# Optimization experiments

Measured on AMD Instinct MI355X. Metric: run time of the kernel, lower is better.

The kernel has to match this reference:

```python
import jax, jax.numpy as jnp
import numpy as np

N_NODES = 100000
N_EDGES = 1000000
D = 64  # gat_input_size == gat_hidden_size
NEG_SLOPE = 0.2  # PyG GATConv default leaky_relu slope


def setup_inputs() -> dict:
    key = jax.random.key(0)
    k1, k2, k3, k4, k5, k6 = jax.random.split(key, 6)
    g = jax.random.normal(k1, (N_NODES, D), dtype=jnp.float32)
    edge_index = jax.random.randint(k2, (2, N_EDGES), 0, N_NODES, dtype=jnp.int32)
    scale = 1.0 / np.sqrt(D)
    W = jax.random.normal(k3, (D, D), dtype=jnp.float32) * scale
    att_src = jax.random.normal(k4, (D,), dtype=jnp.float32) * scale
    att_dst = jax.random.normal(k5, (D,), dtype=jnp.float32) * scale
    bias = jnp.zeros((D,), dtype=jnp.float32)
    return {"g": g, "edge_index": edge_index, "W": W,
            "att_src": att_src, "att_dst": att_dst, "bias": bias}


def _gat_layer(x, src, dst, W, att_src, att_dst, bias):
    N = x.shape[0]
    h = x @ W                               # [N, D] projected features
    a_src = h @ att_src                     # [N] per-node source logits
    a_dst = h @ att_dst                     # [N] per-node target logits
    e = jax.nn.leaky_relu(a_src[src] + a_dst[dst], NEG_SLOPE)  # [E]
    # numerically stable segment softmax over edges grouped by target node
    m = jax.ops.segment_max(e, dst, num_segments=N)            # [N]
    m = jnp.where(jnp.isfinite(m), m, 0.0)                     # isolated nodes
    ex = jnp.exp(e - m[dst])                                   # [E]
    denom = jax.ops.segment_sum(ex, dst, num_segments=N)       # [N]
    alpha = ex / (denom[dst] + 1e-16)                          # [E]
    out = jax.ops.segment_sum(alpha[:, None] * h[src], dst, num_segments=N)
    return out + bias


def reference(g, edge_index, W, att_src, att_dst, bias):
    src, dst = edge_index[0], edge_index[1]
    for _ in range(4):  # same shared GAT applied 4 times
        g = _gat_layer(g, src, dst, W, att_src, att_dst, bias)
    return g
```

## Files before the change

kernel.cpp:

```cpp
#include <hip/hip_runtime.h>
#include <hip/hip_bf16.h>

typedef unsigned int u32;
typedef unsigned short u16;
typedef unsigned long long u64;
typedef __attribute__((ext_vector_type(8))) short short8;
typedef __attribute__((ext_vector_type(4))) float f32x4;
typedef __attribute__((ext_vector_type(2))) float f32x2;

#define LRELU_SLOPE 0.2f
#define BPB 32
#define MAXPER 13000

__device__ inline float bfbits(u32 hi) { union { u32 i; float f; } v; v.i = hi; return v.f; }
__device__ inline float bflo(u32 w) { return bfbits(w << 16); }
__device__ inline float bfhi(u32 w) { return bfbits(w & 0xFFFF0000u); }
__device__ inline float bf2f(u16 s) { return bfbits(((u32)s) << 16); }
__device__ inline u16 f2bf(float f) {
  union { float f; u32 i; } v; v.f = f;
  u32 r = v.i + 0x7FFFu + ((v.i >> 16) & 1u);
  return (u16)(r >> 16);
}
__device__ inline f32x2 up2(u32 w) { return (f32x2){bflo(w), bfhi(w)}; }

__global__ void dp_kernel(const u32* __restrict__ g, int nwords, int* __restrict__ mode,
                          const void* __restrict__ W, const void* __restrict__ as,
                          const void* __restrict__ ad, const void* __restrict__ bs,
                          float* __restrict__ pf, u16* __restrict__ wfrag,
                          int* __restrict__ gcnt) {
  __shared__ int cnt;
  if (threadIdx.x == 0) cnt = 0;
  if (threadIdx.x < 8) gcnt[threadIdx.x] = 0;
  __syncthreads();
  int c = 0;
  for (int i = threadIdx.x; i < nwords; i += 256) {
    u32 e = g[i] & 0x7F80u;
    if (e >= 0x3000u && e <= 0x4180u) c++;
  }
  atomicAdd(&cnt, c);
  __syncthreads();
  int md = (2 * cnt > nwords) ? 1 : 0;
  if (threadIdx.x == 0) *mode = md;

  for (int i = threadIdx.x; i < 4288; i += 256) {
    const void* p; int j;
    if (i < 4096)      { p = W;  j = i; }
    else if (i < 4160) { p = as; j = i - 4096; }
    else if (i < 4224) { p = ad; j = i - 4160; }
    else               { p = bs; j = i - 4224; }
    pf[i] = md ? bf2f(((const u16*)p)[j]) : ((const float*)p)[j];
  }
  __syncthreads();
  for (int i = threadIdx.x; i < 4096; i += 256) {
    int f = i >> 9, lane = (i >> 3) & 63, j = i & 7;
    int cc = f >> 1, t = f & 1;
    int k = 32 * t + 8 * (lane >> 4) + j;
    int n = 16 * cc + (lane & 15);
    wfrag[i] = f2bf(pf[k * 64 + n]);
  }
}

__global__ void __launch_bounds__(256) binA_kernel(
    const int* __restrict__ src, const int* __restrict__ dst, int* __restrict__ gcnt,
    uint2* __restrict__ binned, int E, int nper, int cap) {
  __shared__ int lcnt[8], lbase[8], lcur[8];
  const int K = 8;
  int tile0 = blockIdx.x * (256 * K);
  int t = threadIdx.x;
  if (t < 8) { lcnt[t] = 0; lcur[t] = 0; }
  __syncthreads();
  int dv[K], sv[K], bv[K];
#pragma unroll
  for (int j = 0; j < K; ++j) {
    int idx = tile0 + j * 256 + t;
    bool ok = idx < E;
    int d = ok ? __builtin_nontemporal_load(&dst[idx]) : 0;
    int s = ok ? __builtin_nontemporal_load(&src[idx]) : 0;
    int b = -1;
    if (ok) {
      b = (d >= 4 * nper) ? 4 : 0;
      if (d >= (b + 2) * nper) b += 2;
      if (d >= (b + 1) * nper) b += 1;
      atomicAdd(&lcnt[b], 1);
    }
    dv[j] = d; sv[j] = s; bv[j] = b;
  }
  __syncthreads();
  if (t < 8) lbase[t] = atomicAdd(&gcnt[t], lcnt[t]);
  __syncthreads();
#pragma unroll
  for (int j = 0; j < K; ++j) {
    int b = bv[j];
    if (b >= 0) {
      int slot = lbase[b] + atomicAdd(&lcur[b], 1);
      if (slot < cap) binned[(size_t)b * cap + slot] = make_uint2((u32)sv[j], (u32)dv[j]);
    }
  }
}

__global__ void __launch_bounds__(256) histA_kernel(
    const uint2* __restrict__ binned, const int* __restrict__ gcnt,
    u32* __restrict__ slices, int nper, int cap) {
  __shared__ u32 cnt_lds[MAXPER];
  int b = blockIdx.x & 7;
  int j = blockIdx.x >> 3;
  int cnt = gcnt[b]; if (cnt > cap) cnt = cap;
  int chunk = (cnt + BPB - 1) / BPB;
  int begin = j * chunk;
  int endc = begin + chunk; if (endc > cnt) endc = cnt;
  for (int k = threadIdx.x; k < nper; k += 256) cnt_lds[k] = 0;
  __syncthreads();
  const uint2* reg = binned + (size_t)b * cap;
  int kbase = b * nper;
  for (int i = begin + threadIdx.x; i < endc; i += 256)
    atomicAdd(&cnt_lds[(int)reg[i].y - kbase], 1u);
  __syncthreads();
  u32* out = slices + (size_t)(b * BPB + j) * nper;
  for (int k = threadIdx.x; k < nper; k += 256) out[k] = cnt_lds[k];
}

__global__ void scan1f_kernel(const u32* __restrict__ slices, int* __restrict__ row_off,
                              int* __restrict__ partials, int nper, int N) {
  __shared__ int smem[1024];
  int t = threadIdx.x;
  int idx = blockIdx.x * 1024 + t;
  int v = 0;
  if (idx < N) {
    int b = idx / nper;
    int kk = idx - b * nper;
    const u32* s = slices + (size_t)b * BPB * nper + kk;
    u32 tt = 0;
#pragma unroll 8
    for (int j = 0; j < BPB; ++j) tt += s[(size_t)j * nper];
    v = (int)((tt + 7u) & ~7u);
  }
  smem[t] = v;
  __syncthreads();
  for (int off = 1; off < 1024; off <<= 1) {
    int u = (t >= off) ? smem[t - off] : 0;
    __syncthreads();
    smem[t] += u;
    __syncthreads();
  }
  if (idx < N) row_off[idx + 1] = smem[t];
  if (t == 1023) partials[blockIdx.x] = smem[t];
}

__global__ void scan3c_kernel(int* __restrict__ row_off, const int* __restrict__ partials,
                              int P, u32* __restrict__ slices, int* __restrict__ csr_src,
                              int nper, int N, int dummy) {
  __shared__ int smem[1024];
  int t = threadIdx.x;
  int pv = (t < P) ? partials[t] : 0;
  smem[t] = pv;
  __syncthreads();
  for (int off = 1; off < 1024; off <<= 1) {
    int u = (t >= off) ? smem[t - off] : 0;
    __syncthreads();
    smem[t] += u;
    __syncthreads();
  }
  int blk = blockIdx.x;
  int prefix = (blk > 0) ? smem[blk - 1] : 0;
  int idx = blk * 1024 + t;
  if (idx == 0) row_off[0] = 0;
  if (idx < N) {
    int vend = row_off[idx + 1] + prefix;
    row_off[idx + 1] = vend;
    int b = idx / nper;
    int kk = idx - b * nper;
    u32* s = slices + (size_t)b * BPB * nper + kk;
    u32 tv[BPB];
    u32 deg = 0;
#pragma unroll
    for (int j = 0; j < BPB; ++j) { tv[j] = s[(size_t)j * nper]; deg += tv[j]; }
    u32 pdeg = (deg + 7u) & ~7u;
    u32 run = (u32)vend - pdeg;
#pragma unroll
    for (int j = 0; j < BPB; ++j) { s[(size_t)j * nper] = run; run += tv[j]; }
    for (u32 p = run; p < (u32)vend; ++p) csr_src[p] = dummy;
  }
}

__global__ void __launch_bounds__(256) scatterB_kernel(
    const uint2* __restrict__ binned, const int* __restrict__ gcnt,
    const u32* __restrict__ slices, int* __restrict__ csr_src, int nper, int cap) {
  __shared__ u32 base_lds[MAXPER];
  int b = blockIdx.x & 7;
  int j = blockIdx.x >> 3;
  int cnt = gcnt[b]; if (cnt > cap) cnt = cap;
  int chunk = (cnt + BPB - 1) / BPB;
  int begin = j * chunk;
  int endc = begin + chunk; if (endc > cnt) endc = cnt;
  const u32* s = slices + (size_t)(b * BPB + j) * nper;
  for (int k = threadIdx.x; k < nper; k += 256) base_lds[k] = s[k];
  __syncthreads();
  const uint2* reg = binned + (size_t)b * cap;
  int kbase = b * nper;
  for (int i = begin + threadIdx.x; i < endc; i += 256) {
    uint2 r = reg[i];
    u32 p = atomicAdd(&base_lds[(int)r.y - kbase], 1u);
    csr_src[p] = (int)r.x;
  }
}

__global__ void hist_local_kernel(const uint2* __restrict__ binned, const int* __restrict__ gcnt,
                                  int* __restrict__ deg, int cap) {
  int b = blockIdx.x & 7;
  int vb = blockIdx.x >> 3, nvb = gridDim.x >> 3;
  int cnt = gcnt[b]; if (cnt > cap) cnt = cap;
  const uint2* reg = binned + (size_t)b * cap;
  for (int i = vb * blockDim.x + threadIdx.x; i < cnt; i += nvb * blockDim.x)
    atomicAdd(&deg[reg[i].y], 1);
}

__global__ void scatter_local_kernel(const uint2* __restrict__ binned, const int* __restrict__ gcnt,
                                     int* __restrict__ cursor, int* __restrict__ csr_src, int cap) {
  int b = blockIdx.x & 7;
  int vb = blockIdx.x >> 3, nvb = gridDim.x >> 3;
  int cnt = gcnt[b]; if (cnt > cap) cnt = cap;
  const uint2* reg = binned + (size_t)b * cap;
  for (int i = vb * blockDim.x + threadIdx.x; i < cnt; i += nvb * blockDim.x) {
    uint2 r = reg[i];
    int p = atomicAdd(&cursor[r.y], 1);
    csr_src[p] = (int)r.x;
  }
}

__global__ void scan1_kernel(const int* __restrict__ deg, int* __restrict__ row_off,
                             int* __restrict__ partials, int N) {
  __shared__ int smem[1024];
  int t = threadIdx.x;
  int idx = blockIdx.x * 1024 + t;
  int v = (idx < N) ? (int)(((u32)deg[idx] + 7u) & ~7u) : 0;
  smem[t] = v;
  __syncthreads();
  for (int off = 1; off < 1024; off <<= 1) {
    int u = (t >= off) ? smem[t - off] : 0;
    __syncthreads();
    smem[t] += u;
    __syncthreads();
  }
  if (idx < N) row_off[idx + 1] = smem[t];
  if (t == 1023) partials[blockIdx.x] = smem[t];
}

__global__ void scan2_kernel(int* __restrict__ partials, int P) {
  __shared__ int smem[1024];
  int t = threadIdx.x;
  int v = (t < P) ? partials[t] : 0;
  smem[t] = v;
  __syncthreads();
  for (int off = 1; off < 1024; off <<= 1) {
    int u = (t >= off) ? smem[t - off] : 0;
    __syncthreads();
    smem[t] += u;
    __syncthreads();
  }
  if (t < P) partials[t] = smem[t];
}

__global__ void scan3_kernel(int* __restrict__ row_off, const int* __restrict__ partials,
                             int* __restrict__ cursor, int N) {
  int b = blockIdx.x;
  int idx = b * 1024 + threadIdx.x;
  if (idx < N) {
    int v = row_off[idx + 1] + ((b > 0) ? partials[b - 1] : 0);
    row_off[idx + 1] = v;
    if (idx + 1 < N) cursor[idx + 1] = v;
  }
  if (idx == 0) { row_off[0] = 0; cursor[0] = 0; }
}

__global__ void padC_kernel(const int* __restrict__ row_off, const int* __restrict__ cursor,
                            int* __restrict__ csr_src, int N, int dummy) {
  int i = blockIdx.x * blockDim.x + threadIdx.x;
  if (i >= N) return;
  int e = row_off[i + 1];
  for (int p = cursor[i]; p < e; ++p) csr_src[p] = dummy;
}

__global__ void __launch_bounds__(256) proj0_kernel(
    const void* __restrict__ graw, const int* __restrict__ mode,
    const u16* __restrict__ wfrag, const float* __restrict__ pf,
    u16* __restrict__ h0, u16* __restrict__ h1,
    float* __restrict__ as0, float* __restrict__ as1,
    float* __restrict__ ad0, int N) {
  if (blockIdx.x == 0) {
    if (threadIdx.x < 32)       ((u32*)(h0 + (size_t)N * 64))[threadIdx.x] = 0u;
    else if (threadIdx.x < 64)  ((u32*)(h1 + (size_t)N * 64))[threadIdx.x - 32] = 0u;
    else if (threadIdx.x == 64) as0[N] = -1e30f;
    else if (threadIdx.x == 65) as1[N] = -1e30f;
  }
  int lane = threadIdx.x & 63;
  int quad = lane >> 4, m = lane & 15;
  int wtile = (int)((blockIdx.x * (size_t)blockDim.x + threadIdx.x) >> 6);
  int ntiles = (N + 15) >> 4;
  int nwaves = (int)((gridDim.x * (size_t)blockDim.x) >> 6);

  int md = *mode;
  bool f32in = (md == 0);

  short8 bfrag[8];
#pragma unroll
  for (int f = 0; f < 8; ++f)
    bfrag[f] = *(const short8*)(wfrag + f * 512 + lane * 8);
  float asv[4], adv[4];
#pragma unroll
  for (int c = 0; c < 4; ++c) {
    asv[c] = pf[4096 + 16 * c + m];
    adv[c] = pf[4160 + 16 * c + m];
  }

  for (int tile = wtile; tile < ntiles; tile += nwaves) {
    int row0 = tile << 4;
    int rl = row0 + m; if (rl > N - 1) rl = N - 1;
    short8 a0, a1;
    if (f32in) {
      const float* xr = (const float*)graw + (size_t)rl * 64 + 8 * quad;
      float4 f0 = *(const float4*)(xr);
      float4 f1 = *(const float4*)(xr + 4);
      float4 f2 = *(const float4*)(xr + 32);
      float4 f3 = *(const float4*)(xr + 36);
      a0[0] = (short)f2bf(f0.x); a0[1] = (short)f2bf(f0.y);
      a0[2] = (short)f2bf(f0.z); a0[3] = (short)f2bf(f0.w);
      a0[4] = (short)f2bf(f1.x); a0[5] = (short)f2bf(f1.y);
      a0[6] = (short)f2bf(f1.z); a0[7] = (short)f2bf(f1.w);
      a1[0] = (short)f2bf(f2.x); a1[1] = (short)f2bf(f2.y);
      a1[2] = (short)f2bf(f2.z); a1[3] = (short)f2bf(f2.w);
      a1[4] = (short)f2bf(f3.x); a1[5] = (short)f2bf(f3.y);
      a1[6] = (short)f2bf(f3.z); a1[7] = (short)f2bf(f3.w);
    } else {
      const u16* xr = (const u16*)graw + (size_t)rl * 64 + 8 * quad;
      a0 = *(const short8*)(xr);
      a1 = *(const short8*)(xr + 32);
    }

    f32x4 acc[4];
#pragma unroll
    for (int c = 0; c < 4; ++c) {
      f32x4 z = {0.f, 0.f, 0.f, 0.f};
      z = __builtin_amdgcn_mfma_f32_16x16x32_bf16(a0, bfrag[2 * c + 0], z, 0, 0, 0);
      z = __builtin_amdgcn_mfma_f32_16x16x32_bf16(a1, bfrag[2 * c + 1], z, 0, 0, 0);
      acc[c] = z;
    }

#pragma unroll
    for (int r = 0; r < 4; ++r) {
      int row = row0 + 4 * quad + r;
      float v0 = acc[0][r], v1 = acc[1][r], v2 = acc[2][r], v3 = acc[3][r];
      if (row < N) {
        u16* hr = h0 + (size_t)row * 64 + m;
        hr[0]  = f2bf(v0);
        hr[16] = f2bf(v1);
        hr[32] = f2bf(v2);
        hr[48] = f2bf(v3);
      }
      float s1 = v0 * asv[0] + v1 * asv[1] + v2 * asv[2] + v3 * asv[3];
      float s2 = v0 * adv[0] + v1 * adv[1] + v2 * adv[2] + v3 * adv[3];
#pragma unroll
      for (int msk = 1; msk <= 8; msk <<= 1) {
        s1 += __shfl_xor(s1, msk, 64);
        s2 += __shfl_xor(s2, msk, 64);
      }
      if (m == 0 && row < N) { as0[row] = s1; ad0[row] = s2; }
    }
  }
}

__global__ void __launch_bounds__(256) fusedFG_kernel(
    const u16* __restrict__ hin, const float* __restrict__ asi,
    const float* __restrict__ adi, u16* __restrict__ hout,
    float* __restrict__ aso, float* __restrict__ ado,
    const int* __restrict__ row_off, const int* __restrict__ csr_src,
    const float* __restrict__ pf, const u16* __restrict__ wfrag, int N) {
  __shared__ u16 xs[16][72];
  __shared__ float sred[2][16][4];

  int tid = threadIdx.x;
  int lane = tid & 63;
  int w = tid >> 6;
  int quad = lane >> 4, m = lane & 15;
  int grp = lane >> 4;
  int eg = (lane >> 3) & 1;
  int fg = lane & 7;
  int tile = blockIdx.x;
  int row_in = w * 4 + grp;
  int i = tile * 16 + row_in;
  bool valid = i < N;

  short8 bf0 = *(const short8*)(wfrag + (2 * w + 0) * 512 + lane * 8);
  short8 bf1 = *(const short8*)(wfrag + (2 * w + 1) * 512 + lane * 8);
  float asw = pf[4096 + 16 * w + m];
  float adw = pf[4160 + 16 * w + m];

  int beg = 0, end = 0;
  float advv = 0.f;
  if (valid) { beg = row_off[i]; end = row_off[i + 1]; advv = adi[i]; }

  f32x2 acc0 = {0.f, 0.f}, acc1 = {0.f, 0.f}, acc2 = {0.f, 0.f}, acc3 = {0.f, 0.f};
  float den = 0.f;
  for (int b0 = beg; b0 < end; b0 += 8) {
    int eA = b0 + eg;
    int sA = csr_src[eA];
    int sB = csr_src[eA + 2];
    int sC = csr_src[eA + 4];
    int sD = csr_src[eA + 6];
    float aA = asi[sA];
    float aB = asi[sB];
    float aC = asi[sC];
    float aD = asi[sD];
    uint4 hA = ((const uint4*)(hin + (size_t)sA * 64))[fg];
    uint4 hB = ((const uint4*)(hin + (size_t)sB * 64))[fg];
    uint4 hC = ((const uint4*)(hin + (size_t)sC * 64))[fg];
    uint4 hD = ((const uint4*)(hin + (size_t)sD * 64))[fg];

    float tA = aA + advv; tA = (tA > 0.f) ? tA : LRELU_SLOPE * tA;
    float tB = aB + advv; tB = (tB > 0.f) ? tB : LRELU_SLOPE * tB;
    float tC = aC + advv; tC = (tC > 0.f) ? tC : LRELU_SLOPE * tC;
    float tD = aD + advv; tD = (tD > 0.f) ? tD : LRELU_SLOPE * tD;
    float wA = __expf(fminf(tA, 60.f));
    float wB = __expf(fminf(tB, 60.f));
    float wC = __expf(fminf(tC, 60.f));
    float wD = __expf(fminf(tD, 60.f));
    den += (wA + wB) + (wC + wD);
    f32x2 wA2 = {wA, wA}, wB2 = {wB, wB}, wC2 = {wC, wC}, wD2 = {wD, wD};
    acc0 += wA2 * up2(hA.x); acc0 += wB2 * up2(hB.x);
    acc0 += wC2 * up2(hC.x); acc0 += wD2 * up2(hD.x);
    acc1 += wA2 * up2(hA.y); acc1 += wB2 * up2(hB.y);
    acc1 += wC2 * up2(hC.y); acc1 += wD2 * up2(hD.y);
    acc2 += wA2 * up2(hA.z); acc2 += wB2 * up2(hB.z);
    acc2 += wC2 * up2(hC.z); acc2 += wD2 * up2(hD.z);
    acc3 += wA2 * up2(hA.w); acc3 += wB2 * up2(hB.w);
    acc3 += wC2 * up2(hC.w); acc3 += wD2 * up2(hD.w);
  }
  den += __shfl_xor(den, 8, 64);
#pragma unroll
  for (int c = 0; c < 2; ++c) {
    acc0[c] += __shfl_xor(acc0[c], 8, 64);
    acc1[c] += __shfl_xor(acc1[c], 8, 64);
    acc2[c] += __shfl_xor(acc2[c], 8, 64);
    acc3[c] += __shfl_xor(acc3[c], 8, 64);
  }
  float inv = (den > 0.f) ? 1.f / den : 0.f;
  float oa[8] = {acc0[0], acc0[1], acc1[0], acc1[1],
                 acc2[0], acc2[1], acc3[0], acc3[1]};

  if (!eg) {
    u32 o[4];
    if (valid) {
#pragma unroll
      for (int j = 0; j < 4; ++j) {
        float v0 = oa[2 * j]     * inv + pf[4224 + 8 * fg + 2 * j];
        float v1 = oa[2 * j + 1] * inv + pf[4224 + 8 * fg + 2 * j + 1];
        o[j] = (u32)f2bf(v0) | ((u32)f2bf(v1) << 16);
      }
    } else {
      o[0] = o[1] = o[2] = o[3] = 0u;
    }
    *(uint4*)&xs[row_in][fg * 8] = make_uint4(o[0], o[1], o[2], o[3]);
  }
  __syncthreads();

  short8 a0 = *(const short8*)&xs[m][8 * quad];
  short8 a1 = *(const short8*)&xs[m][32 + 8 * quad];
  f32x4 z = {0.f, 0.f, 0.f, 0.f};
  z = __builtin_amdgcn_mfma_f32_16x16x32_bf16(a0, bf0, z, 0, 0, 0);
  z = __builtin_amdgcn_mfma_f32_16x16x32_bf16(a1, bf1, z, 0, 0, 0);
#pragma unroll
  for (int r = 0; r < 4; ++r) {
    int row = tile * 16 + 4 * quad + r;
    if (row < N) hout[(size_t)row * 64 + 16 * w + m] = f2bf(z[r]);
    float s1 = z[r] * asw, s2 = z[r] * adw;
#pragma unroll
    for (int msk = 1; msk <= 8; msk <<= 1) {
      s1 += __shfl_xor(s1, msk, 64);
      s2 += __shfl_xor(s2, msk, 64);
    }
    if (m == 0) { sred[0][4 * quad + r][w] = s1; sred[1][4 * quad + r][w] = s2; }
  }
  __syncthreads();
  if (tid < 32) {
    int row = tid & 15, sel = tid >> 4;
    float v = sred[sel][row][0] + sred[sel][row][1] + sred[sel][row][2] + sred[sel][row][3];
    int gr = tile * 16 + row;
    if (gr < N) (sel ? ado : aso)[gr] = v;
  }
}

__global__ void __launch_bounds__(256) gatherL_kernel(
    const u16* __restrict__ h, const float* __restrict__ a_src,
    const float* __restrict__ a_dst, const int* __restrict__ row_off,
    const int* __restrict__ csr_src, const float* __restrict__ pf,
    void* __restrict__ dout, int N, const int* __restrict__ mode) {
  int lane = threadIdx.x & 63;
  int grp = lane >> 4;
  int eg  = (lane >> 3) & 1;
  int fg  = lane & 7;
  int wid = (int)((blockIdx.x * blockDim.x + threadIdx.x) >> 6);
  int i0 = wid * 4;
  if (i0 >= N) return;
  int i = i0 + grp;
  bool valid = i < N;

  int beg = 0, end = 0;
  float adv = 0.f;
  if (valid) {
    beg = row_off[i];
    end = row_off[i + 1];
    adv = a_dst[i];
  }

  f32x2 acc0 = {0.f, 0.f}, acc1 = {0.f, 0.f}, acc2 = {0.f, 0.f}, acc3 = {0.f, 0.f};
  float den = 0.f;

  for (int b0 = beg; b0 < end; b0 += 8) {
    int eA = b0 + eg;
    int sA = csr_src[eA];
    int sB = csr_src[eA + 2];
    int sC = csr_src[eA + 4];
    int sD = csr_src[eA + 6];
    float aA = a_src[sA];
    float aB = a_src[sB];
    float aC = a_src[sC];
    float aD = a_src[sD];
    uint4 hA = ((const uint4*)(h + (size_t)sA * 64))[fg];
    uint4 hB = ((const uint4*)(h + (size_t)sB * 64))[fg];
    uint4 hC = ((const uint4*)(h + (size_t)sC * 64))[fg];
    uint4 hD = ((const uint4*)(h + (size_t)sD * 64))[fg];

    float tA = aA + adv; tA = (tA > 0.f) ? tA : LRELU_SLOPE * tA;
    float tB = aB + adv; tB = (tB > 0.f) ? tB : LRELU_SLOPE * tB;
    float tC = aC + adv; tC = (tC > 0.f) ? tC : LRELU_SLOPE * tC;
    float tD = aD + adv; tD = (tD > 0.f) ? tD : LRELU_SLOPE * tD;
    float wA = __expf(fminf(tA, 60.f));
    float wB = __expf(fminf(tB, 60.f));
    float wC = __expf(fminf(tC, 60.f));
    float wD = __expf(fminf(tD, 60.f));
    den += (wA + wB) + (wC + wD);
    f32x2 wA2 = {wA, wA}, wB2 = {wB, wB}, wC2 = {wC, wC}, wD2 = {wD, wD};
    acc0 += wA2 * up2(hA.x); acc0 += wB2 * up2(hB.x);
    acc0 += wC2 * up2(hC.x); acc0 += wD2 * up2(hD.x);
    acc1 += wA2 * up2(hA.y); acc1 += wB2 * up2(hB.y);
    acc1 += wC2 * up2(hC.y); acc1 += wD2 * up2(hD.y);
    acc2 += wA2 * up2(hA.z); acc2 += wB2 * up2(hB.z);
    acc2 += wC2 * up2(hC.z); acc2 += wD2 * up2(hD.z);
    acc3 += wA2 * up2(hA.w); acc3 += wB2 * up2(hB.w);
    acc3 += wC2 * up2(hC.w); acc3 += wD2 * up2(hD.w);
  }

  den += __shfl_xor(den, 8, 64);
#pragma unroll
  for (int c = 0; c < 2; ++c) {
    acc0[c] += __shfl_xor(acc0[c], 8, 64);
    acc1[c] += __shfl_xor(acc1[c], 8, 64);
    acc2[c] += __shfl_xor(acc2[c], 8, 64);
    acc3[c] += __shfl_xor(acc3[c], 8, 64);
  }
  float inv = (den > 0.f) ? 1.f / den : 0.f;

  if (!valid || eg) return;

  float oa[8] = {acc0[0], acc0[1], acc1[0], acc1[1], acc2[0], acc2[1], acc3[0], acc3[1]};
  if (*mode) {
    u32 o[4];
#pragma unroll
    for (int j = 0; j < 4; ++j) {
      float f0 = oa[2 * j]     * inv + pf[4224 + 8 * fg + 2 * j];
      float f1 = oa[2 * j + 1] * inv + pf[4224 + 8 * fg + 2 * j + 1];
      o[j] = (u32)f2bf(f0) | ((u32)f2bf(f1) << 16);
    }
    *(uint4*)((u16*)dout + (size_t)i * 64 + fg * 8) = make_uint4(o[0], o[1], o[2], o[3]);
  } else {
    float o[8];
#pragma unroll
    for (int j = 0; j < 8; ++j)
      o[j] = oa[j] * inv + pf[4224 + 8 * fg + j];
    float* dp = (float*)dout + (size_t)i * 64 + fg * 8;
    *(float4*)(dp)     = make_float4(o[0], o[1], o[2], o[3]);
    *(float4*)(dp + 4) = make_float4(o[4], o[5], o[6], o[7]);
  }
}

extern "C" void kernel_launch(void* const* d_in, const int* in_sizes, int n_in,
                              void* d_out, int out_size, void* d_ws, size_t ws_size,
                              hipStream_t stream) {
  const void* g     = d_in[0];
  const int*  edge  = (const int*)d_in[1];
  const void* Wp    = d_in[2];
  const void* attsp = d_in[3];
  const void* attdp = d_in[4];
  const void* biasp = d_in[5];

  const int D = 64;
  const int N = in_sizes[0] / D;
  const int E = in_sizes[1] / 2;
  const int* src = edge;
  const int* dst = edge + E;

  int nper = (N + 7) / 8;
  bool fast_csr = (nper <= MAXPER);

  char* ws = (char*)d_ws;
  size_t off = 0;
  auto alloc = [&](size_t bytes) -> char* {
    char* p = ws + off;
    off += (bytes + 255) & ~size_t(255);
    return p;
  };
  size_t h_bytes = (size_t)(N + 1) * D * sizeof(u16);
  size_t slice_bytes = (size_t)8 * BPB * nper * sizeof(u32);
  u16*   h0       = (u16*)alloc(h_bytes > slice_bytes ? h_bytes : slice_bytes);
  u16*   h1       = (u16*)alloc(h_bytes);
  u32*   slices   = (u32*)h0;
  float* pf       = (float*)alloc(4288 * sizeof(float));
  u16*   wfrag    = (u16*)alloc(4096 * sizeof(u16));
  float* as0      = (float*)alloc((size_t)(N + 1) * sizeof(float));
  float* as1      = (float*)alloc((size_t)(N + 1) * sizeof(float));
  float* ad0      = (float*)alloc((size_t)N * sizeof(float));
  float* ad1      = (float*)alloc((size_t)N * sizeof(float));
  int*   deg      = (int*)alloc((size_t)N * sizeof(int));
  int*   row_off  = (int*)alloc((size_t)(N + 1) * sizeof(int));
  int*   cursor   = (int*)alloc((size_t)N * sizeof(int));
  int*   csr_src  = (int*)alloc(((size_t)E + 8 * (size_t)N) * sizeof(int));
  int*   partials = (int*)alloc(1024 * sizeof(int));
  int*   mode     = (int*)alloc(256);
  int*   gcnt     = (int*)alloc(256);
  int    cap      = E / 8 + 16384;
  uint2* binned   = (uint2*)alloc((size_t)8 * cap * sizeof(uint2));

  dp_kernel<<<1, 256, 0, stream>>>((const u32*)g, 4096, mode, Wp, attsp, attdp, biasp,
                                   pf, wfrag, gcnt);

  if (!fast_csr) hipMemsetAsync(deg, 0, (size_t)N * sizeof(int), stream);
  int abl = (E + 2047) / 2048;
  binA_kernel<<<abl, 256, 0, stream>>>(src, dst, gcnt, binned, E, nper, cap);

  int nblk = (N + 1023) / 1024;
  if (fast_csr) {
    histA_kernel<<<8 * BPB, 256, 0, stream>>>(binned, gcnt, slices, nper, cap);
    scan1f_kernel<<<nblk, 1024, 0, stream>>>(slices, row_off, partials, nper, N);
    scan3c_kernel<<<nblk, 1024, 0, stream>>>(row_off, partials, nblk, slices, csr_src,
                                             nper, N, N);
    scatterB_kernel<<<8 * BPB, 256, 0, stream>>>(binned, gcnt, slices, csr_src, nper, cap);
  } else {
    hist_local_kernel<<<1024, 256, 0, stream>>>(binned, gcnt, deg, cap);
    scan1_kernel<<<nblk, 1024, 0, stream>>>(deg, row_off, partials, N);
    scan2_kernel<<<1, 1024, 0, stream>>>(partials, nblk);
    scan3_kernel<<<nblk, 1024, 0, stream>>>(row_off, partials, cursor, N);
    scatter_local_kernel<<<1024, 256, 0, stream>>>(binned, gcnt, cursor, csr_src, cap);
    padC_kernel<<<(N + 255) / 256, 256, 0, stream>>>(row_off, cursor, csr_src, N, N);
  }

  int ntiles = (N + 15) / 16;
  int tblocks = (ntiles + 3) / 4;

  proj0_kernel<<<tblocks, 256, 0, stream>>>(g, mode, wfrag, pf, h0, h1, as0, as1, ad0, N);

  fusedFG_kernel<<<ntiles, 256, 0, stream>>>(h0, as0, ad0, h1, as1, ad1,
                                             row_off, csr_src, pf, wfrag, N);
  fusedFG_kernel<<<ntiles, 256, 0, stream>>>(h1, as1, ad1, h0, as0, ad0,
                                             row_off, csr_src, pf, wfrag, N);
  fusedFG_kernel<<<ntiles, 256, 0, stream>>>(h0, as0, ad0, h1, as1, ad1,
                                             row_off, csr_src, pf, wfrag, N);

  gatherL_kernel<<<ntiles, 256, 0, stream>>>(h1, as1, ad1, row_off, csr_src, pf,
                                             d_out, N, mode);
}
```

Measured before the change: 267.8 us.

## Fuse edge binning with first projection and add XCD-aware tile swizzle

Edge binning and the layer-0 projection now run as one launch, with the block ranges split between the two jobs. This lets independent work overlap and removes a launch. To make that possible, the slices buffer no longer aliases h0 and gets its own allocation. The fused aggregation and final gather kernels remap block IDs so that consecutive tiles land on the same XCD, which should improve L2 locality. The gather kernel's indexing also changes to one 16-row tile per block. The cost is extra workspace memory and some imbalance between the two kinds of block inside the fused launch.

New measurement: 261.2 us (median of 2 runs). -2.5%, faster.

```diff
diff --git a/kernel.cpp b/kernel.cpp
--- a/kernel.cpp
+++ b/kernel.cpp
@@ -23,6 +23,12 @@
 }
 __device__ inline f32x2 up2(u32 w) { return (f32x2){bflo(w), bfhi(w)}; }
 
+__device__ inline int xcd_swz(int orig, int nwg) {
+  int xcd = orig & 7, idx = orig >> 3;
+  int q = nwg >> 3, r = nwg & 7;
+  return (xcd < r ? xcd * (q + 1) : r * (q + 1) + (xcd - r) * q) + idx;
+}
+
 __global__ void dp_kernel(const u32* __restrict__ g, int nwords, int* __restrict__ mode,
                           const void* __restrict__ W, const void* __restrict__ as,
                           const void* __restrict__ ad, const void* __restrict__ bs,
@@ -60,12 +66,12 @@
   }
 }
 
-__global__ void __launch_bounds__(256) binA_kernel(
-    const int* __restrict__ src, const int* __restrict__ dst, int* __restrict__ gcnt,
-    uint2* __restrict__ binned, int E, int nper, int cap) {
+__device__ void binA_body(const int* __restrict__ src, const int* __restrict__ dst,
+                          int* __restrict__ gcnt, uint2* __restrict__ binned,
+                          int E, int nper, int cap, int bid) {
   __shared__ int lcnt[8], lbase[8], lcur[8];
   const int K = 8;
-  int tile0 = blockIdx.x * (256 * K);
+  int tile0 = bid * (256 * K);
   int t = threadIdx.x;
   if (t < 8) { lcnt[t] = 0; lcur[t] = 0; }
   __syncthreads();
@@ -98,195 +104,12 @@
   }
 }
 
-__global__ void __launch_bounds__(256) histA_kernel(
-    const uint2* __restrict__ binned, const int* __restrict__ gcnt,
-    u32* __restrict__ slices, int nper, int cap) {
-  __shared__ u32 cnt_lds[MAXPER];
-  int b = blockIdx.x & 7;
-  int j = blockIdx.x >> 3;
-  int cnt = gcnt[b]; if (cnt > cap) cnt = cap;
-  int chunk = (cnt + BPB - 1) / BPB;
-  int begin = j * chunk;
-  int endc = begin + chunk; if (endc > cnt) endc = cnt;
-  for (int k = threadIdx.x; k < nper; k += 256) cnt_lds[k] = 0;
-  __syncthreads();
-  const uint2* reg = binned + (size_t)b * cap;
-  int kbase = b * nper;
-  for (int i = begin + threadIdx.x; i < endc; i += 256)
-    atomicAdd(&cnt_lds[(int)reg[i].y - kbase], 1u);
-  __syncthreads();
-  u32* out = slices + (size_t)(b * BPB + j) * nper;
-  for (int k = threadIdx.x; k < nper; k += 256) out[k] = cnt_lds[k];
-}
-
-__global__ void scan1f_kernel(const u32* __restrict__ slices, int* __restrict__ row_off,
-                              int* __restrict__ partials, int nper, int N) {
-  __shared__ int smem[1024];
-  int t = threadIdx.x;
-  int idx = blockIdx.x * 1024 + t;
-  int v = 0;
-  if (idx < N) {
-    int b = idx / nper;
-    int kk = idx - b * nper;
-    const u32* s = slices + (size_t)b * BPB * nper + kk;
-    u32 tt = 0;
-#pragma unroll 8
-    for (int j = 0; j < BPB; ++j) tt += s[(size_t)j * nper];
-    v = (int)((tt + 7u) & ~7u);
-  }
-  smem[t] = v;
-  __syncthreads();
-  for (int off = 1; off < 1024; off <<= 1) {
-    int u = (t >= off) ? smem[t - off] : 0;
-    __syncthreads();
-    smem[t] += u;
-    __syncthreads();
-  }
-  if (idx < N) row_off[idx + 1] = smem[t];
-  if (t == 1023) partials[blockIdx.x] = smem[t];
-}
-
-__global__ void scan3c_kernel(int* __restrict__ row_off, const int* __restrict__ partials,
-                              int P, u32* __restrict__ slices, int* __restrict__ csr_src,
-                              int nper, int N, int dummy) {
-  __shared__ int smem[1024];
-  int t = threadIdx.x;
-  int pv = (t < P) ? partials[t] : 0;
-  smem[t] = pv;
-  __syncthreads();
-  for (int off = 1; off < 1024; off <<= 1) {
-    int u = (t >= off) ? smem[t - off] : 0;
-    __syncthreads();
-    smem[t] += u;
-    __syncthreads();
-  }
-  int blk = blockIdx.x;
-  int prefix = (blk > 0) ? smem[blk - 1] : 0;
-  int idx = blk * 1024 + t;
-  if (idx == 0) row_off[0] = 0;
-  if (idx < N) {
-    int vend = row_off[idx + 1] + prefix;
-    row_off[idx + 1] = vend;
-    int b = idx / nper;
-    int kk = idx - b * nper;
-    u32* s = slices + (size_t)b * BPB * nper + kk;
-    u32 tv[BPB];
-    u32 deg = 0;
-#pragma unroll
-    for (int j = 0; j < BPB; ++j) { tv[j] = s[(size_t)j * nper]; deg += tv[j]; }
-    u32 pdeg = (deg + 7u) & ~7u;
-    u32 run = (u32)vend - pdeg;
-#pragma unroll
-    for (int j = 0; j < BPB; ++j) { s[(size_t)j * nper] = run; run += tv[j]; }
-    for (u32 p = run; p < (u32)vend; ++p) csr_src[p] = dummy;
-  }
-}
-
-__global__ void __launch_bounds__(256) scatterB_kernel(
-    const uint2* __restrict__ binned, const int* __restrict__ gcnt,
-    const u32* __restrict__ slices, int* __restrict__ csr_src, int nper, int cap) {
-  __shared__ u32 base_lds[MAXPER];
-  int b = blockIdx.x & 7;
-  int j = blockIdx.x >> 3;
-  int cnt = gcnt[b]; if (cnt > cap) cnt = cap;
-  int chunk = (cnt + BPB - 1) / BPB;
-  int begin = j * chunk;
-  int endc = begin + chunk; if (endc > cnt) endc = cnt;
-  const u32* s = slices + (size_t)(b * BPB + j) * nper;
-  for (int k = threadIdx.x; k < nper; k += 256) base_lds[k] = s[k];
-  __syncthreads();
-  const uint2* reg = binned + (size_t)b * cap;
-  int kbase = b * nper;
-  for (int i = begin + threadIdx.x; i < endc; i += 256) {
-    uint2 r = reg[i];
-    u32 p = atomicAdd(&base_lds[(int)r.y - kbase], 1u);
-    csr_src[p] = (int)r.x;
-  }
-}
-
-__global__ void hist_local_kernel(const uint2* __restrict__ binned, const int* __restrict__ gcnt,
-                                  int* __restrict__ deg, int cap) {
-  int b = blockIdx.x & 7;
-  int vb = blockIdx.x >> 3, nvb = gridDim.x >> 3;
-  int cnt = gcnt[b]; if (cnt > cap) cnt = cap;
-  const uint2* reg = binned + (size_t)b * cap;
-  for (int i = vb * blockDim.x + threadIdx.x; i < cnt; i += nvb * blockDim.x)
-    atomicAdd(&deg[reg[i].y], 1);
-}
-
-__global__ void scatter_local_kernel(const uint2* __restrict__ binned, const int* __restrict__ gcnt,
-                                     int* __restrict__ cursor, int* __restrict__ csr_src, int cap) {
-  int b = blockIdx.x & 7;
-  int vb = blockIdx.x >> 3, nvb = gridDim.x >> 3;
-  int cnt = gcnt[b]; if (cnt > cap) cnt = cap;
-  const uint2* reg = binned + (size_t)b * cap;
-  for (int i = vb * blockDim.x + threadIdx.x; i < cnt; i += nvb * blockDim.x) {
-    uint2 r = reg[i];
-    int p = atomicAdd(&cursor[r.y], 1);
-    csr_src[p] = (int)r.x;
-  }
-}
-
-__global__ void scan1_kernel(const int* __restrict__ deg, int* __restrict__ row_off,
-                             int* __restrict__ partials, int N) {
-  __shared__ int smem[1024];
-  int t = threadIdx.x;
-  int idx = blockIdx.x * 1024 + t;
-  int v = (idx < N) ? (int)(((u32)deg[idx] + 7u) & ~7u) : 0;
-  smem[t] = v;
-  __syncthreads();
-  for (int off = 1; off < 1024; off <<= 1) {
-    int u = (t >= off) ? smem[t - off] : 0;
-    __syncthreads();
-    smem[t] += u;
-    __syncthreads();
-  }
-  if (idx < N) row_off[idx + 1] = smem[t];
-  if (t == 1023) partials[blockIdx.x] = smem[t];
-}
-
-__global__ void scan2_kernel(int* __restrict__ partials, int P) {
-  __shared__ int smem[1024];
-  int t = threadIdx.x;
-  int v = (t < P) ? partials[t] : 0;
-  smem[t] = v;
-  __syncthreads();
-  for (int off = 1; off < 1024; off <<= 1) {
-    int u = (t >= off) ? smem[t - off] : 0;
-    __syncthreads();
-    smem[t] += u;
-    __syncthreads();
-  }
-  if (t < P) partials[t] = smem[t];
-}
-
-__global__ void scan3_kernel(int* __restrict__ row_off, const int* __restrict__ partials,
-                             int* __restrict__ cursor, int N) {
-  int b = blockIdx.x;
-  int idx = b * 1024 + threadIdx.x;
-  if (idx < N) {
-    int v = row_off[idx + 1] + ((b > 0) ? partials[b - 1] : 0);
-    row_off[idx + 1] = v;
-    if (idx + 1 < N) cursor[idx + 1] = v;
-  }
-  if (idx == 0) { row_off[0] = 0; cursor[0] = 0; }
-}
-
-__global__ void padC_kernel(const int* __restrict__ row_off, const int* __restrict__ cursor,
-                            int* __restrict__ csr_src, int N, int dummy) {
-  int i = blockIdx.x * blockDim.x + threadIdx.x;
-  if (i >= N) return;
-  int e = row_off[i + 1];
-  for (int p = cursor[i]; p < e; ++p) csr_src[p] = dummy;
-}
-
-__global__ void __launch_bounds__(256) proj0_kernel(
-    const void* __restrict__ graw, const int* __restrict__ mode,
-    const u16* __restrict__ wfrag, const float* __restrict__ pf,
-    u16* __restrict__ h0, u16* __restrict__ h1,
-    float* __restrict__ as0, float* __restrict__ as1,
-    float* __restrict__ ad0, int N) {
-  if (blockIdx.x == 0) {
+__device__ void proj0_body(const void* __restrict__ graw, const int* __restrict__ mode,
+                           const u16* __restrict__ wfrag, const float* __restrict__ pf,
+                           u16* __restrict__ h0, u16* __restrict__ h1,
+                           float* __restrict__ as0, float* __restrict__ as1,
+                           float* __restrict__ ad0, int N, int bid, int pblocks) {
+  if (bid == 0) {
     if (threadIdx.x < 32)       ((u32*)(h0 + (size_t)N * 64))[threadIdx.x] = 0u;
     else if (threadIdx.x < 64)  ((u32*)(h1 + (size_t)N * 64))[threadIdx.x - 32] = 0u;
     else if (threadIdx.x == 64) as0[N] = -1e30f;
@@ -294,9 +117,9 @@
   }
   int lane = threadIdx.x & 63;
   int quad = lane >> 4, m = lane & 15;
-  int wtile = (int)((blockIdx.x * (size_t)blockDim.x + threadIdx.x) >> 6);
+  int wtile = (int)(((size_t)bid * 256 + threadIdx.x) >> 6);
   int ntiles = (N + 15) >> 4;
-  int nwaves = (int)((gridDim.x * (size_t)blockDim.x) >> 6);
+  int nwaves = pblocks * 4;
 
   int md = *mode;
   bool f32in = (md == 0);
@@ -368,6 +191,219 @@
   }
 }
 
+__global__ void __launch_bounds__(256) fatBP_kernel(
+    const int* __restrict__ src, const int* __restrict__ dst, int* __restrict__ gcnt,
+    uint2* __restrict__ binned, int E, int nper, int cap, int abl,
+    const void* __restrict__ graw, const int* __restrict__ mode,
+    const u16* __restrict__ wfrag, const float* __restrict__ pf,
+    u16* __restrict__ h0, u16* __restrict__ h1,
+    float* __restrict__ as0, float* __restrict__ as1,
+    float* __restrict__ ad0, int N) {
+  if ((int)blockIdx.x < abl) {
+    binA_body(src, dst, gcnt, binned, E, nper, cap, (int)blockIdx.x);
+  } else {
+    proj0_body(graw, mode, wfrag, pf, h0, h1, as0, as1, ad0, N,
+               (int)blockIdx.x - abl, (int)gridDim.x - abl);
+  }
+}
+
+__global__ void __launch_bounds__(256) binA_kernel(
+    const int* __restrict__ src, const int* __restrict__ dst, int* __restrict__ gcnt,
+    uint2* __restrict__ binned, int E, int nper, int cap) {
+  binA_body(src, dst, gcnt, binned, E, nper, cap, (int)blockIdx.x);
+}
+__global__ void __launch_bounds__(256) proj0_kernel(
+    const void* __restrict__ graw, const int* __restrict__ mode,
+    const u16* __restrict__ wfrag, const float* __restrict__ pf,
+    u16* __restrict__ h0, u16* __restrict__ h1,
+    float* __restrict__ as0, float* __restrict__ as1,
+    float* __restrict__ ad0, int N) {
+  proj0_body(graw, mode, wfrag, pf, h0, h1, as0, as1, ad0, N,
+             (int)blockIdx.x, (int)gridDim.x);
+}
+
+__global__ void __launch_bounds__(256) histA_kernel(
+    const uint2* __restrict__ binned, const int* __restrict__ gcnt,
+    u32* __restrict__ slices, int nper, int cap) {
+  __shared__ u32 cnt_lds[MAXPER];
+  int b = blockIdx.x & 7;
+  int j = blockIdx.x >> 3;
+  int cnt = gcnt[b]; if (cnt > cap) cnt = cap;
+  int chunk = (cnt + BPB - 1) / BPB;
+  int begin = j * chunk;
+  int endc = begin + chunk; if (endc > cnt) endc = cnt;
+  for (int k = threadIdx.x; k < nper; k += 256) cnt_lds[k] = 0;
+  __syncthreads();
+  const uint2* reg = binned + (size_t)b * cap;
+  int kbase = b * nper;
+  for (int i = begin + threadIdx.x; i < endc; i += 256)
+    atomicAdd(&cnt_lds[(int)reg[i].y - kbase], 1u);
+  __syncthreads();
+  u32* out = slices + (size_t)(b * BPB + j) * nper;
+  for (int k = threadIdx.x; k < nper; k += 256) out[k] = cnt_lds[k];
+}
+
+__global__ void scan1f_kernel(const u32* __restrict__ slices, int* __restrict__ row_off,
+                              int* __restrict__ partials, int nper, int N) {
+  __shared__ int smem[1024];
+  int t = threadIdx.x;
+  int idx = blockIdx.x * 1024 + t;
+  int v = 0;
+  if (idx < N) {
+    int b = idx / nper;
+    int kk = idx - b * nper;
+    const u32* s = slices + (size_t)b * BPB * nper + kk;
+    u32 tt = 0;
+#pragma unroll 8
+    for (int j = 0; j < BPB; ++j) tt += s[(size_t)j * nper];
+    v = (int)((tt + 7u) & ~7u);
+  }
+  smem[t] = v;
+  __syncthreads();
+  for (int off = 1; off < 1024; off <<= 1) {
+    int u = (t >= off) ? smem[t - off] : 0;
+    __syncthreads();
+    smem[t] += u;
+    __syncthreads();
+  }
+  if (idx < N) row_off[idx + 1] = smem[t];
+  if (t == 1023) partials[blockIdx.x] = smem[t];
+}
+
+__global__ void scan3c_kernel(int* __restrict__ row_off, const int* __restrict__ partials,
+                              int P, u32* __restrict__ slices, int* __restrict__ csr_src,
+                              int nper, int N, int dummy) {
+  __shared__ int smem[1024];
+  int t = threadIdx.x;
+  int pv = (t < P) ? partials[t] : 0;
+  smem[t] = pv;
+  __syncthreads();
+  for (int off = 1; off < 1024; off <<= 1) {
+    int u = (t >= off) ? smem[t - off] : 0;
+    __syncthreads();
+    smem[t] += u;
+    __syncthreads();
+  }
+  int blk = blockIdx.x;
+  int prefix = (blk > 0) ? smem[blk - 1] : 0;
+  int idx = blk * 1024 + t;
+  if (idx == 0) row_off[0] = 0;
+  if (idx < N) {
+    int vend = row_off[idx + 1] + prefix;
+    row_off[idx + 1] = vend;
+    int b = idx / nper;
+    int kk = idx - b * nper;
+    u32* s = slices + (size_t)b * BPB * nper + kk;
+    u32 tv[BPB];
+    u32 deg = 0;
+#pragma unroll
+    for (int j = 0; j < BPB; ++j) { tv[j] = s[(size_t)j * nper]; deg += tv[j]; }
+    u32 pdeg = (deg + 7u) & ~7u;
+    u32 run = (u32)vend - pdeg;
+#pragma unroll
+    for (int j = 0; j < BPB; ++j) { s[(size_t)j * nper] = run; run += tv[j]; }
+    for (u32 p = run; p < (u32)vend; ++p) csr_src[p] = dummy;
+  }
+}
+
+__global__ void __launch_bounds__(256) scatterB_kernel(
+    const uint2* __restrict__ binned, const int* __restrict__ gcnt,
+    const u32* __restrict__ slices, int* __restrict__ csr_src, int nper, int cap) {
+  __shared__ u32 base_lds[MAXPER];
+  int b = blockIdx.x & 7;
+  int j = blockIdx.x >> 3;
+  int cnt = gcnt[b]; if (cnt > cap) cnt = cap;
+  int chunk = (cnt + BPB - 1) / BPB;
+  int begin = j * chunk;
+  int endc = begin + chunk; if (endc > cnt) endc = cnt;
+  const u32* s = slices + (size_t)(b * BPB + j) * nper;
+  for (int k = threadIdx.x; k < nper; k += 256) base_lds[k] = s[k];
+  __syncthreads();
+  const uint2* reg = binned + (size_t)b * cap;
+  int kbase = b * nper;
+  for (int i = begin + threadIdx.x; i < endc; i += 256) {
+    uint2 r = reg[i];
+    u32 p = atomicAdd(&base_lds[(int)r.y - kbase], 1u);
+    csr_src[p] = (int)r.x;
+  }
+}
+
+__global__ void hist_local_kernel(const uint2* __restrict__ binned, const int* __restrict__ gcnt,
+                                  int* __restrict__ deg, int cap) {
+  int b = blockIdx.x & 7;
+  int vb = blockIdx.x >> 3, nvb = gridDim.x >> 3;
+  int cnt = gcnt[b]; if (cnt > cap) cnt = cap;
+  const uint2* reg = binned + (size_t)b * cap;
+  for (int i = vb * blockDim.x + threadIdx.x; i < cnt; i += nvb * blockDim.x)
+    atomicAdd(&deg[reg[i].y], 1);
+}
+
+__global__ void scatter_local_kernel(const uint2* __restrict__ binned, const int* __restrict__ gcnt,
+                                     int* __restrict__ cursor, int* __restrict__ csr_src, int cap) {
+  int b = blockIdx.x & 7;
+  int vb = blockIdx.x >> 3, nvb = gridDim.x >> 3;
+  int cnt = gcnt[b]; if (cnt > cap) cnt = cap;
+  const uint2* reg = binned + (size_t)b * cap;
+  for (int i = vb * blockDim.x + threadIdx.x; i < cnt; i += nvb * blockDim.x) {
+    uint2 r = reg[i];
+    int p = atomicAdd(&cursor[r.y], 1);
+    csr_src[p] = (int)r.x;
+  }
+}
+
+__global__ void scan1_kernel(const int* __restrict__ deg, int* __restrict__ row_off,
+                             int* __restrict__ partials, int N) {
+  __shared__ int smem[1024];
+  int t = threadIdx.x;
+  int idx = blockIdx.x * 1024 + t;
+  int v = (idx < N) ? (int)(((u32)deg[idx] + 7u) & ~7u) : 0;
+  smem[t] = v;
+  __syncthreads();
+  for (int off = 1; off < 1024; off <<= 1) {
+    int u = (t >= off) ? smem[t - off] : 0;
+    __syncthreads();
+    smem[t] += u;
+    __syncthreads();
+  }
+  if (idx < N) row_off[idx + 1] = smem[t];
+  if (t == 1023) partials[blockIdx.x] = smem[t];
+}
+
+__global__ void scan2_kernel(int* __restrict__ partials, int P) {
+  __shared__ int smem[1024];
+  int t = threadIdx.x;
+  int v = (t < P) ? partials[t] : 0;
+  smem[t] = v;
+  __syncthreads();
+  for (int off = 1; off < 1024; off <<= 1) {
+    int u = (t >= off) ? smem[t - off] : 0;
+    __syncthreads();
+    smem[t] += u;
+    __syncthreads();
+  }
+  if (t < P) partials[t] = smem[t];
+}
+
+__global__ void scan3_kernel(int* __restrict__ row_off, const int* __restrict__ partials,
+                             int* __restrict__ cursor, int N) {
+  int b = blockIdx.x;
+  int idx = b * 1024 + threadIdx.x;
+  if (idx < N) {
+    int v = row_off[idx + 1] + ((b > 0) ? partials[b - 1] : 0);
+    row_off[idx + 1] = v;
+    if (idx + 1 < N) cursor[idx + 1] = v;
+  }
+  if (idx == 0) { row_off[0] = 0; cursor[0] = 0; }
+}
+
+__global__ void padC_kernel(const int* __restrict__ row_off, const int* __restrict__ cursor,
+                            int* __restrict__ csr_src, int N, int dummy) {
+  int i = blockIdx.x * blockDim.x + threadIdx.x;
+  if (i >= N) return;
+  int e = row_off[i + 1];
+  for (int p = cursor[i]; p < e; ++p) csr_src[p] = dummy;
+}
+
 __global__ void __launch_bounds__(256) fusedFG_kernel(
     const u16* __restrict__ hin, const float* __restrict__ asi,
     const float* __restrict__ adi, u16* __restrict__ hout,
@@ -384,7 +420,7 @@
   int grp = lane >> 4;
   int eg = (lane >> 3) & 1;
   int fg = lane & 7;
-  int tile = blockIdx.x;
+  int tile = xcd_swz((int)blockIdx.x, (int)gridDim.x);
   int row_in = w * 4 + grp;
   int i = tile * 16 + row_in;
   bool valid = i < N;
@@ -497,10 +533,9 @@
   int grp = lane >> 4;
   int eg  = (lane >> 3) & 1;
   int fg  = lane & 7;
-  int wid = (int)((blockIdx.x * blockDim.x + threadIdx.x) >> 6);
-  int i0 = wid * 4;
-  if (i0 >= N) return;
-  int i = i0 + grp;
+  int w   = threadIdx.x >> 6;
+  int tile = xcd_swz((int)blockIdx.x, (int)gridDim.x);
+  int i = tile * 16 + w * 4 + grp;
   bool valid = i < N;
 
   int beg = 0, end = 0;
@@ -609,10 +644,9 @@
     return p;
   };
   size_t h_bytes = (size_t)(N + 1) * D * sizeof(u16);
-  size_t slice_bytes = (size_t)8 * BPB * nper * sizeof(u32);
-  u16*   h0       = (u16*)alloc(h_bytes > slice_bytes ? h_bytes : slice_bytes);
+  u16*   h0       = (u16*)alloc(h_bytes);
   u16*   h1       = (u16*)alloc(h_bytes);
-  u32*   slices   = (u32*)h0;
+  u32*   slices   = (u32*)alloc((size_t)8 * BPB * nper * sizeof(u32));
   float* pf       = (float*)alloc(4288 * sizeof(float));
   u16*   wfrag    = (u16*)alloc(4096 * sizeof(u16));
   float* as0      = (float*)alloc((size_t)(N + 1) * sizeof(float));
@@ -634,28 +668,29 @@
 
   if (!fast_csr) hipMemsetAsync(deg, 0, (size_t)N * sizeof(int), stream);
   int abl = (E + 2047) / 2048;
-  binA_kernel<<<abl, 256, 0, stream>>>(src, dst, gcnt, binned, E, nper, cap);
+  int ntiles = (N + 15) / 16;
+  int tblocks = (ntiles + 3) / 4;
 
   int nblk = (N + 1023) / 1024;
   if (fast_csr) {
+    fatBP_kernel<<<abl + tblocks, 256, 0, stream>>>(
+        src, dst, gcnt, binned, E, nper, cap, abl,
+        g, mode, wfrag, pf, h0, h1, as0, as1, ad0, N);
     histA_kernel<<<8 * BPB, 256, 0, stream>>>(binned, gcnt, slices, nper, cap);
     scan1f_kernel<<<nblk, 1024, 0, stream>>>(slices, row_off, partials, nper, N);
     scan3c_kernel<<<nblk, 1024, 0, stream>>>(row_off, partials, nblk, slices, csr_src,
                                              nper, N, N);
     scatterB_kernel<<<8 * BPB, 256, 0, stream>>>(binned, gcnt, slices, csr_src, nper, cap);
   } else {
+    binA_kernel<<<abl, 256, 0, stream>>>(src, dst, gcnt, binned, E, nper, cap);
     hist_local_kernel<<<1024, 256, 0, stream>>>(binned, gcnt, deg, cap);
     scan1_kernel<<<nblk, 1024, 0, stream>>>(deg, row_off, partials, N);
     scan2_kernel<<<1, 1024, 0, stream>>>(partials, nblk);
     scan3_kernel<<<nblk, 1024, 0, stream>>>(row_off, partials, cursor, N);
     scatter_local_kernel<<<1024, 256, 0, stream>>>(binned, gcnt, cursor, csr_src, cap);
     padC_kernel<<<(N + 255) / 256, 256, 0, stream>>>(row_off, cursor, csr_src, N, N);
-  }
-
-  int ntiles = (N + 15) / 16;
-  int tblocks = (ntiles + 3) / 4;
-
-  proj0_kernel<<<tblocks, 256, 0, stream>>>(g, mode, wfrag, pf, h0, h1, as0, as1, ad0, N);
+    proj0_kernel<<<tblocks, 256, 0, stream>>>(g, mode, wfrag, pf, h0, h1, as0, as1, ad0, N);
+  }
 
   fusedFG_kernel<<<ntiles, 256, 0, stream>>>(h0, as0, ad0, h1, as1, ad1,
                                              row_off, csr_src, pf, wfrag, N);
```
